# Optimization experiments

Measured on AMD Instinct MI355X. Metric: run time of the kernel, lower is better.

Reference implementation:

```python
import jax, jax.numpy as jnp
import numpy as np

HIDDEN = 2048
N_HEADS = 16
N_KV = 4
HEAD_DIM = 128
SEQ = 2048
BATCH = 2
THETA = 10000.0


def rotate_half(x):
    half = x.shape[-1] // 2
    x1, x2 = x[..., :half], x[..., half:]
    return jnp.concatenate((-x2, x1), axis=-1)


def rope_cos_sin(seq_len, dim, theta, dtype):
    inv_freq = 1.0 / (theta ** (jnp.arange(0, dim, 2, dtype=jnp.float32) / dim))
    t = jnp.arange(seq_len, dtype=jnp.float32)
    freqs = jnp.einsum('i,j->ij', t, inv_freq)            # [S, dim/2]
    emb = jnp.concatenate((freqs, freqs), axis=-1)        # [S, dim]
    return jnp.cos(emb).astype(dtype), jnp.sin(emb).astype(dtype)


def setup_inputs() -> dict:
    key = jax.random.key(0)
    kx, kq, kk, kv, ko = jax.random.split(key, 5)
    s = 0.02
    return {
        'x':  jax.random.normal(kx, (BATCH, SEQ, HIDDEN), dtype=jnp.float32),
        'Wq': jax.random.normal(kq, (HIDDEN, N_HEADS * HEAD_DIM), dtype=jnp.float32) * s,
        'Wk': jax.random.normal(kk, (HIDDEN, N_KV * HEAD_DIM), dtype=jnp.float32) * s,
        'Wv': jax.random.normal(kv, (HIDDEN, N_KV * HEAD_DIM), dtype=jnp.float32) * s,
        'Wo': jax.random.normal(ko, (N_HEADS * HEAD_DIM, HIDDEN), dtype=jnp.float32) * s,
    }


def reference(x, Wq, Wk, Wv, Wo):
    B, S, _ = x.shape
    q = (x @ Wq).reshape(B, S, N_HEADS, HEAD_DIM)
    k = (x @ Wk).reshape(B, S, N_KV, HEAD_DIM)
    v = (x @ Wv).reshape(B, S, N_KV, HEAD_DIM)

    cos, sin = rope_cos_sin(S, HEAD_DIM, THETA, x.dtype)
    cos = cos[None, :, None, :]  # [1,S,1,D]
    sin = sin[None, :, None, :]
    q = q * cos + rotate_half(q) * sin
    k = k * cos + rotate_half(k) * sin

    repeat = N_HEADS // N_KV
    k = jnp.repeat(k, repeat, axis=2)  # repeat_interleave over heads
    v = jnp.repeat(v, repeat, axis=2)

    # [B,H,S,D]
    q = q.transpose(0, 2, 1, 3)
    k = k.transpose(0, 2, 1, 3)
    v = v.transpose(0, 2, 1, 3)

    scale = HEAD_DIM ** -0.5
    scores = jnp.einsum('bhqd,bhkd->bhqk', q, k) * scale
    causal = jnp.triu(jnp.full((S, S), -jnp.inf, dtype=scores.dtype), k=1)
    scores = scores + causal
    probs = jax.nn.softmax(scores, axis=-1)
    out = jnp.einsum('bhqk,bhkd->bhqd', probs, v)
    out = out.transpose(0, 2, 1, 3).reshape(B, S, N_HEADS * HEAD_DIM)
    return out @ Wo
```

## Files before the change

kernel.cpp:

```cpp
#include <hip/hip_runtime.h>
#include <hip/hip_bf16.h>
#include <math.h>

#define HIDDEN 2048
#define NHEADS 16
#define NKV 4
#define HD 128
#define SEQ 2048
#define BATCH 2
#define MTOT (BATCH*SEQ)
#define NQ (NHEADS*HD)
#define NKVD (NKV*HD)
#define NQKV (NQ + 2*NKVD)

typedef __attribute__((ext_vector_type(8))) short short8;
typedef __attribute__((ext_vector_type(4))) float float4v;

#if __has_builtin(__builtin_amdgcn_exp2f)
#define EXP2F __builtin_amdgcn_exp2f
#else
#define EXP2F exp2f
#endif
#define C1 0.1275174f

static __device__ __forceinline__ unsigned short f2bf(float f) {
  union { float f; unsigned int u; } v; v.f = f;
  unsigned int r = v.u + 0x7FFF + ((v.u >> 16) & 1);
  return (unsigned short)(r >> 16);
}
static __device__ __forceinline__ float bf2f(unsigned short h) {
  union { unsigned int u; float f; } v; v.u = ((unsigned int)h) << 16;
  return v.f;
}

static __device__ __forceinline__ void async16(const unsigned short* g, unsigned short* l) {
  __builtin_amdgcn_global_load_lds(
      (const __attribute__((address_space(1))) unsigned int*)g,
      (__attribute__((address_space(3))) unsigned int*)l, 16, 0, 0);
}

__global__ void prep(const float* __restrict__ x, unsigned short* __restrict__ xb,
                     const float* __restrict__ Wq, const float* __restrict__ Wk,
                     const float* __restrict__ Wv, const float* __restrict__ Wo,
                     unsigned short* __restrict__ Wqt, unsigned short* __restrict__ Wkt,
                     unsigned short* __restrict__ Wvt, unsigned short* __restrict__ Wot) {
  __shared__ float tile[32][33];
  int bx = blockIdx.x;
  if (bx < 8192) {
    int i = (bx * 256 + threadIdx.x) * 4;
    float4 v = *(const float4*)(x + i);
    ushort4 o;
    o.x = f2bf(v.x); o.y = f2bf(v.y); o.z = f2bf(v.z); o.w = f2bf(v.w);
    *(ushort4*)(xb + i) = o;
    return;
  }
  int bz = bx - 8192;
  int tbx = bz % 160, tby = bz / 160;
  const int K = 2048;
  const float* W; unsigned short* Wt; int N; int tn;
  if (tbx < 64)      { W = Wq; Wt = Wqt; N = NQ;     tn = tbx * 32; }
  else if (tbx < 80) { W = Wk; Wt = Wkt; N = NKVD;   tn = (tbx - 64) * 32; }
  else if (tbx < 96) { W = Wv; Wt = Wvt; N = NKVD;   tn = (tbx - 80) * 32; }
  else               { W = Wo; Wt = Wot; N = HIDDEN; tn = (tbx - 96) * 32; }
  int tk = tby * 32;
  int tx = threadIdx.x & 31;
  int ty = threadIdx.x >> 5;
  #pragma unroll
  for (int i = 0; i < 4; i++) {
    int k = tk + ty + i * 8;
    tile[ty + i * 8][tx] = W[(size_t)k * N + tn + tx];
  }
  __syncthreads();
  #pragma unroll
  for (int i = 0; i < 4; i++) {
    int n = tn + ty + i * 8;
    Wt[(size_t)n * K + tk + tx] = f2bf(tile[tx][ty + i * 8]);
  }
}

__global__ void rope_k(unsigned short* __restrict__ Kb) {
  int idx = blockIdx.x * blockDim.x + threadIdx.x;
  int d = idx & 63;
  int hr = idx >> 6;
  int spos = (hr / NKV) % SEQ;
  size_t base = (size_t)hr * HD;
  float inv = exp2f((float)d * -0.2076205059304601f);
  float ang = (float)spos * inv;
  float sn, cs;
  sincosf(ang, &sn, &cs);
  float q1 = bf2f(Kb[base + d]);
  float q2 = bf2f(Kb[base + d + 64]);
  Kb[base + d]      = f2bf(q1 * cs - q2 * sn);
  Kb[base + d + 64] = f2bf(q2 * cs + q1 * sn);
}

__global__ __launch_bounds__(1024, 4) void gemm_qkv(
    const unsigned short* __restrict__ A,
    const unsigned short* __restrict__ Bt,
    unsigned short* __restrict__ Qb,
    unsigned short* __restrict__ Kb,
    unsigned short* __restrict__ Vt) {
  __shared__ __align__(16) unsigned short L[4 * 16384];
  const int K = HIDDEN;
  const int NT = K / 32;
  int bm = blockIdx.y * 256, bn = blockIdx.x * 256;
  int tid = threadIdx.x, w = tid >> 6, lane = tid & 63;
  int wrow = w >> 2, wcol = w & 3;
  int m16 = lane & 15, quad = lane >> 4;
  int r = tid >> 2, lch = tid & 3;
  int lchs = lch ^ ((r >> 1) & 3);
  int qx = quad ^ ((m16 >> 1) & 3);
  const unsigned short* Agp = A + (size_t)(bm + r) * K + lchs * 8;
  const unsigned short* Bgp = Bt + (size_t)(bn + r) * K + lchs * 8;

  float4v acc[4][4];
  #pragma unroll
  for (int i = 0; i < 4; i++)
    #pragma unroll
    for (int j = 0; j < 4; j++) acc[i][j] = (float4v)0.0f;

  auto stage = [&](int t) {
    unsigned short* Lb = L + (t & 3) * 16384;
    int k0 = t * 32;
    async16(Agp + k0, Lb + tid * 8);
    async16(Bgp + k0, Lb + 8192 + tid * 8);
  };

  const bool isV = (blockIdx.x >= 10);

  stage(0); stage(1);
  asm volatile("s_waitcnt vmcnt(2)" ::: "memory");
  __builtin_amdgcn_s_barrier();
  __builtin_amdgcn_sched_barrier(0);

  if (!isV) {
    for (int t = 0; t < NT; ++t) {
      if (t + 2 < NT) stage(t + 2);
      const unsigned short* Ab_ = L + (t & 3) * 16384;
      const unsigned short* Bb_ = Ab_ + 8192;
      short8 af[4], bfr[4];
      #pragma unroll
      for (int i = 0; i < 4; i++)
        af[i] = *(const short8*)(&Ab_[(wrow * 64 + i * 16 + m16) * 32 + qx * 8]);
      #pragma unroll
      for (int j = 0; j < 4; j++)
        bfr[j] = *(const short8*)(&Bb_[(wcol * 64 + j * 16 + m16) * 32 + qx * 8]);
      __builtin_amdgcn_s_setprio(1);
      #pragma unroll
      for (int i = 0; i < 4; i++)
        #pragma unroll
        for (int j = 0; j < 4; j++)
          acc[i][j] = __builtin_amdgcn_mfma_f32_16x16x32_bf16(af[i], bfr[j], acc[i][j], 0, 0, 0);
      __builtin_amdgcn_s_setprio(0);
      if (t + 2 < NT) { asm volatile("s_waitcnt vmcnt(2)" ::: "memory"); }
      else            { asm volatile("s_waitcnt vmcnt(0)" ::: "memory"); }
      __builtin_amdgcn_s_barrier();
      __builtin_amdgcn_sched_barrier(0);
    }
  } else {
    for (int t = 0; t < NT; ++t) {
      if (t + 2 < NT) stage(t + 2);
      const unsigned short* Ab_ = L + (t & 3) * 16384;
      const unsigned short* Bb_ = Ab_ + 8192;
      short8 af[4], bfr[4];
      #pragma unroll
      for (int i = 0; i < 4; i++)
        af[i] = *(const short8*)(&Ab_[(wrow * 64 + i * 16 + m16) * 32 + qx * 8]);
      #pragma unroll
      for (int j = 0; j < 4; j++)
        bfr[j] = *(const short8*)(&Bb_[(wcol * 64 + j * 16 + m16) * 32 + qx * 8]);
      __builtin_amdgcn_s_setprio(1);
      #pragma unroll
      for (int i = 0; i < 4; i++)
        #pragma unroll
        for (int j = 0; j < 4; j++)
          acc[i][j] = __builtin_amdgcn_mfma_f32_16x16x32_bf16(bfr[j], af[i], acc[i][j], 0, 0, 0);
      __builtin_amdgcn_s_setprio(0);
      if (t + 2 < NT) { asm volatile("s_waitcnt vmcnt(2)" ::: "memory"); }
      else            { asm volatile("s_waitcnt vmcnt(0)" ::: "memory"); }
      __builtin_amdgcn_s_barrier();
      __builtin_amdgcn_sched_barrier(0);
    }
  }

  if (blockIdx.x < 8) {
    #pragma unroll
    for (int i = 0; i < 4; i++)
      #pragma unroll
      for (int j = 0; j < 4; j++)
        #pragma unroll
        for (int rr = 0; rr < 4; rr++) {
          int row = bm + wrow * 64 + i * 16 + quad * 4 + rr;
          int col = bn + wcol * 64 + j * 16 + m16;
          Qb[(size_t)row * NQ + col] = f2bf(acc[i][j][rr]);
        }
  } else if (!isV) {
    #pragma unroll
    for (int i = 0; i < 4; i++)
      #pragma unroll
      for (int j = 0; j < 4; j++)
        #pragma unroll
        for (int rr = 0; rr < 4; rr++) {
          int row = bm + wrow * 64 + i * 16 + quad * 4 + rr;
          int col = bn - 2048 + wcol * 64 + j * 16 + m16;
          Kb[(size_t)row * NKVD + col] = f2bf(acc[i][j][rr]);
        }
  } else {
    #pragma unroll
    for (int i = 0; i < 4; i++)
      #pragma unroll
      for (int j = 0; j < 4; j++)
        #pragma unroll
        for (int rr = 0; rr < 4; rr++) {
          int f = bn - 2560 + wcol * 64 + j * 16 + quad * 4 + rr;
          int m = bm + wrow * 64 + i * 16 + m16;
          Vt[(size_t)f * MTOT + m] = f2bf(acc[i][j][rr]);
        }
  }
}

__global__ __launch_bounds__(512, 4) void gemm_o(
    const unsigned short* __restrict__ A,
    const unsigned short* __restrict__ Bt,
    float* __restrict__ C, int M, int N, int K) {
  __shared__ __align__(16) unsigned short L[4 * 8192];
  const int NT = K / 32;
  int bm = blockIdx.y * 128, bn = blockIdx.x * 128;
  int tid = threadIdx.x, w = tid >> 6, lane = tid & 63;
  int wrow = w >> 2, wcol = w & 3;
  int m16 = lane & 15, quad = lane >> 4;
  int r = tid >> 2, lch = tid & 3;
  int lchs = lch ^ ((r >> 1) & 3);
  int qx = quad ^ ((m16 >> 1) & 3);
  const unsigned short* Agp = A + (size_t)(bm + r) * K + lchs * 8;
  const unsigned short* Bgp = Bt + (size_t)(bn + r) * K + lchs * 8;

  float4v acc[4][2];
  #pragma unroll
  for (int i = 0; i < 4; i++)
    #pragma unroll
    for (int j = 0; j < 2; j++) acc[i][j] = (float4v)0.0f;

  auto stage = [&](int t) {
    unsigned short* Lb = L + (t & 3) * 8192;
    int k0 = t * 32;
    async16(Agp + k0, Lb + tid * 8);
    async16(Bgp + k0, Lb + 4096 + tid * 8);
  };

  stage(0); stage(1);
  asm volatile("s_waitcnt vmcnt(2)" ::: "memory");
  __builtin_amdgcn_s_barrier();
  __builtin_amdgcn_sched_barrier(0);

  for (int t = 0; t < NT; ++t) {
    if (t + 2 < NT) stage(t + 2);
    const unsigned short* Ab_ = L + (t & 3) * 8192;
    const unsigned short* Bb_ = Ab_ + 4096;
    short8 af[4], bfr[2];
    #pragma unroll
    for (int i = 0; i < 4; i++)
      af[i] = *(const short8*)(&Ab_[(wrow * 64 + i * 16 + m16) * 32 + qx * 8]);
    #pragma unroll
    for (int j = 0; j < 2; j++)
      bfr[j] = *(const short8*)(&Bb_[(wcol * 32 + j * 16 + m16) * 32 + qx * 8]);
    __builtin_amdgcn_s_setprio(1);
    #pragma unroll
    for (int i = 0; i < 4; i++)
      #pragma unroll
      for (int j = 0; j < 2; j++)
        acc[i][j] = __builtin_amdgcn_mfma_f32_16x16x32_bf16(af[i], bfr[j], acc[i][j], 0, 0, 0);
    __builtin_amdgcn_s_setprio(0);
    if (t + 2 < NT) { asm volatile("s_waitcnt vmcnt(2)" ::: "memory"); }
    else            { asm volatile("s_waitcnt vmcnt(0)" ::: "memory"); }
    __builtin_amdgcn_s_barrier();
    __builtin_amdgcn_sched_barrier(0);
  }

  #pragma unroll
  for (int i = 0; i < 4; i++)
    #pragma unroll
    for (int j = 0; j < 2; j++)
      #pragma unroll
      for (int rr = 0; rr < 4; rr++) {
        int row = bm + wrow * 64 + i * 16 + quad * 4 + rr;
        int col = bn + wcol * 32 + j * 16 + m16;
        C[(size_t)row * N + col] = acc[i][j][rr];
      }
}

#define FLASH_TILE(CUR, NXT)                                                  \
  {                                                                           \
    const int ktb = kt * 64;                                                  \
    __syncthreads();        \
    {                                                                         \
      const unsigned short* Vg = Vt + vgrow * (size_t)MTOT                    \
                                    + (size_t)b * SEQ + ktb + kcv * 32 + vlch * 8; \
      unsigned short* Vl = Vs + kcv * 4096 + ipv * 512;                       \
      _Pragma("unroll")                                                       \
      for (int i = 0; i < 4; i++) async16(Vg + (size_t)i * 16 * MTOT, Vl + i * 512); \
    }                                                                         \
    if (kt < H) {                                                             \
      const unsigned short* Kg = Kp + (((size_t)b * SEQ + (kt + 1) * 64 + lrow) * NKV + kvh) * HD + w * 32 + vlch * 8; \
      unsigned short* Kl = NXT + w * 2048;                                    \
      _Pragma("unroll")                                                       \
      for (int i = 0; i < 4; i++) async16(Kg + (size_t)i * 16 * NKV * HD, Kl + i * 512); \
    }                                                                         \
    const bool act1 = (ktb <= lmax_w);                                        \
    float4v sacc[2][4];                                                       \
    _Pragma("unroll") for (int s4 = 0; s4 < 4; s4++) {                        \
      sacc[0][s4] = (float4v)0.0f; sacc[1][s4] = (float4v)0.0f; }             \
    __builtin_amdgcn_s_setprio(1);                                            \
    if (act1) {                                                               \
      _Pragma("unroll")                                                       \
      for (int s4 = 0; s4 < 4; s4++)                                          \
        _Pragma("unroll")                                                     \
        for (int c = 0; c < 4; c++) {                                         \
          short8 kf = *(const short8*)(&CUR[c * 2048 + (s4 * 16 + m16) * 32 + qx * 8]); \
          sacc[0][s4] = __builtin_amdgcn_mfma_f32_16x16x32_bf16(kf, qf[0][c], sacc[0][s4], 0, 0, 0); \
          sacc[1][s4] = __builtin_amdgcn_mfma_f32_16x16x32_bf16(kf, qf[1][c], sacc[1][s4], 0, 0, 0); \
        }                                                                     \
    } else {                                                                  \
      _Pragma("unroll")                                                       \
      for (int s4 = 0; s4 < 4; s4++)                                          \
        _Pragma("unroll")                                                     \
        for (int c = 0; c < 4; c++) {                                         \
          short8 kf = *(const short8*)(&CUR[c * 2048 + (s4 * 16 + m16) * 32 + qx * 8]); \
          sacc[0][s4] = __builtin_amdgcn_mfma_f32_16x16x32_bf16(kf, qf[0][c], sacc[0][s4], 0, 0, 0); \
        }                                                                     \
    }                                                                         \
    __builtin_amdgcn_s_setprio(0);                                            \
    _Pragma("unroll")                                                         \
    for (int qs = 0; qs < 2; qs++) {                                          \
      if (qs == 0 || act1) {                                                  \
        const int tb = qs ? L : H;                                            \
        const int qabs = tb * 64 + w * 16 + m16;                              \
        const bool diag = (kt == tb);                                         \
        float sv[4][4]; float mloc = -1e30f;                                  \
        if (diag) {                                                           \
          _Pragma("unroll") for (int s4 = 0; s4 < 4; s4++)                    \
            _Pragma("unroll") for (int rr = 0; rr < 4; rr++) {                \
              int kabs = ktb + s4 * 16 + quad * 4 + rr;                       \
              float t = sacc[qs][s4][rr];                                     \
              sv[s4][rr] = (kabs > qabs) ? -1e30f : t;                        \
              mloc = fmaxf(mloc, sv[s4][rr]); }                               \
        } else {                                                              \
          _Pragma("unroll") for (int s4 = 0; s4 < 4; s4++)                    \
            _Pragma("unroll") for (int rr = 0; rr < 4; rr++) {                \
              sv[s4][rr] = sacc[qs][s4][rr]; mloc = fmaxf(mloc, sv[s4][rr]); } \
        }                                                                     \
        mloc *= C1;                                                           \
        mloc = fmaxf(mloc, __shfl_xor(mloc, 16, 64));                         \
        mloc = fmaxf(mloc, __shfl_xor(mloc, 32, 64));                         \
        float mnewS = fmaxf(miS[qs], mloc);                                   \
        const bool defer = (bool)__all(mloc <= miS[qs] + 8.0f);               \
        if (defer) mnewS = miS[qs];  \
        const int prow = qs * 64 + w * 16 + m16;                              \
        const int psw = prow * 32; const int rx = prow & 7;                   \
        float rs = 0.0f;                                                      \
        _Pragma("unroll") for (int s4 = 0; s4 < 4; s4++) {                    \
          float p0 = EXP2F(__builtin_fmaf(sv[s4][0], C1, -mnewS));            \
          float p1 = EXP2F(__builtin_fmaf(sv[s4][1], C1, -mnewS));            \
          float p2 = EXP2F(__builtin_fmaf(sv[s4][2], C1, -mnewS));            \
          float p3 = EXP2F(__builtin_fmaf(sv[s4][3], C1, -mnewS));            \
          rs += p0 + p1 + p2 + p3;                                            \
          uint2 u;                                                            \
          u.x = (__float_as_uint(p1) & 0xffff0000u) | (__float_as_uint(p0) >> 16); \
          u.y = (__float_as_uint(p3) & 0xffff0000u) | (__float_as_uint(p2) >> 16); \
          int chunkW = s4 * 2 + (quad >> 1);                                  \
          *(uint2*)(&Ps[psw + ((chunkW ^ rx) << 2) + (quad & 1) * 2]) = u;    \
        }                                                                     \
        rs += __shfl_xor(rs, 16, 64);                                         \
        rs += __shfl_xor(rs, 32, 64);                                         \
        if (!defer) {                                                         \
          const float alpha = EXP2F(miS[qs] - mnewS);                         \
          li[qs] *= alpha; miS[qs] = mnewS;                                   \
          _Pragma("unroll") for (int ds = 0; ds < 8; ds++) oacc[ds][qs] *= alpha; \
        }                                                                     \
        li[qs] += rs;                                                         \
      }                                                                       \
    }                                                                         \
    __syncthreads();     \
    {                                                                         \
      const int r0 = w * 16 + m16, r1 = 64 + w * 16 + m16;                    \
      __builtin_amdgcn_s_setprio(1);                                          \
      if (act1) {                                                             \
        _Pragma("unroll")                                                     \
        for (int kc = 0; kc < 2; kc++) {                                      \
          short8 pf0 = *(const short8*)(&Ps[r0 * 32 + (((kc * 4 + quad) ^ (r0 & 7)) << 2)]); \
          short8 pf1 = *(const short8*)(&Ps[r1 * 32 + (((kc * 4 + quad) ^ (r1 & 7)) << 2)]); \
          _Pragma("unroll")                                                   \
          for (int ds = 0; ds < 8; ds++) {                                    \
            short8 vf = *(const short8*)(&Vs[kc * 4096 + (ds * 16 + m16) * 32 + qx * 8]); \
            oacc[ds][0] = __builtin_amdgcn_mfma_f32_16x16x32_bf16(vf, pf0, oacc[ds][0], 0, 0, 0); \
            oacc[ds][1] = __builtin_amdgcn_mfma_f32_16x16x32_bf16(vf, pf1, oacc[ds][1], 0, 0, 0); \
          }                                                                   \
        }                                                                     \
      } else {                                                                \
        _Pragma("unroll")                                                     \
        for (int kc = 0; kc < 2; kc++) {                                      \
          short8 pf0 = *(const short8*)(&Ps[r0 * 32 + (((kc * 4 + quad) ^ (r0 & 7)) << 2)]); \
          _Pragma("unroll")                                                   \
          for (int ds = 0; ds < 8; ds++) {                                    \
            short8 vf = *(const short8*)(&Vs[kc * 4096 + (ds * 16 + m16) * 32 + qx * 8]); \
            oacc[ds][0] = __builtin_amdgcn_mfma_f32_16x16x32_bf16(vf, pf0, oacc[ds][0], 0, 0, 0); \
          }                                                                   \
        }                                                                     \
      }                                                                       \
      __builtin_amdgcn_s_setprio(0);                                          \
    }                                                                         \
  }

__global__ __launch_bounds__(256, 2) void flash_attn(
    const unsigned short* __restrict__ Q,
    const unsigned short* __restrict__ Kp,
    const unsigned short* __restrict__ Vt,
    unsigned short* __restrict__ O) {
  __shared__ unsigned short Ks0[4 * 64 * 32];
  __shared__ unsigned short Ks1[4 * 64 * 32];
  __shared__ unsigned short Vs[2 * 128 * 32];
  __shared__ unsigned int   Ps[128 * 32];

  int bx = blockIdx.x;
  int h  = blockIdx.y;
  int b  = blockIdx.z;
  int kvh = h >> 2;
  int H = 31 - bx, L = bx;
  int tid = threadIdx.x;
  int w = tid >> 6, lane = tid & 63;
  int m16 = lane & 15, quad = lane >> 4;
  int lrow = lane >> 2, lch = lane & 3;
  const int vlch = lch ^ ((lrow >> 1) & 3);
  const int qx = quad ^ ((m16 >> 1) & 3);
  const int lmax_w = L * 64 + w * 16 + 15;

  const int kcv = w >> 1, ipv = (w & 1) * 4;
  const size_t vgrow = (size_t)kvh * HD + ipv * 16 + lrow;

  short8 qf[2][4];
  #pragma unroll
  for (int qs = 0; qs < 2; qs++) {
    int tb = qs ? L : H;
    size_t qbase = (((size_t)b * SEQ + tb * 64 + w * 16 + m16) * NHEADS + h) * HD;
    #pragma unroll
    for (int c = 0; c < 4; c++)
      qf[qs][c] = *(const short8*)(Q + qbase + c * 32 + quad * 8);
  }
  #pragma unroll
  for (int qs = 0; qs < 2; qs++) {
    int tb = qs ? L : H;
    float spos = (float)(tb * 64 + w * 16 + m16);
    #pragma unroll
    for (int c = 0; c < 2; c++) {
      #pragma unroll
      for (int e = 0; e < 8; e++) {
        int d = c * 32 + quad * 8 + e;
        float inv = exp2f((float)d * -0.2076205059304601f);
        float ang = spos * inv;
        float sn, cs;
        sincosf(ang, &sn, &cs);
        float f1 = bf2f((unsigned short)qf[qs][c][e]);
        float f2 = bf2f((unsigned short)qf[qs][c + 2][e]);
        qf[qs][c][e]     = (short)f2bf(f1 * cs - f2 * sn);
        qf[qs][c + 2][e] = (short)f2bf(f2 * cs + f1 * sn);
      }
    }
  }

  float4v oacc[8][2];
  #pragma unroll
  for (int ds = 0; ds < 8; ds++) { oacc[ds][0] = (float4v)0.0f; oacc[ds][1] = (float4v)0.0f; }
  float miS[2] = {-1e30f, -1e30f}, li[2] = {0.0f, 0.0f};

  {
    const unsigned short* Kg = Kp + (((size_t)b * SEQ + lrow) * NKV + kvh) * HD + w * 32 + vlch * 8;
    unsigned short* Kl = Ks0 + w * 2048;
    #pragma unroll
    for (int i = 0; i < 4; i++) async16(Kg + (size_t)i * 16 * NKV * HD, Kl + i * 512);
  }

  int kt = 0;
  for (;;) {
    FLASH_TILE(Ks0, Ks1)
    if (++kt > H) break;
    FLASH_TILE(Ks1, Ks0)
    if (++kt > H) break;
  }

  #pragma unroll
  for (int qs = 0; qs < 2; qs++) {
    float inv = 1.0f / li[qs];
    int tb = qs ? L : H;
    int qabs = tb * 64 + w * 16 + m16;
    size_t obase = (((size_t)b * SEQ + qabs) * NHEADS + h) * HD + quad * 4;
    #pragma unroll
    for (int ds = 0; ds < 8; ds++) {
      float v0 = oacc[ds][qs][0] * inv;
      float v1 = oacc[ds][qs][1] * inv;
      float v2 = oacc[ds][qs][2] * inv;
      float v3 = oacc[ds][qs][3] * inv;
      uint2 u;
      u.x = ((unsigned)f2bf(v1) << 16) | f2bf(v0);
      u.y = ((unsigned)f2bf(v3) << 16) | f2bf(v2);
      *(uint2*)(O + obase + ds * 16) = u;
    }
  }
}

extern "C" void kernel_launch(void* const* d_in, const int* in_sizes, int n_in,
                              void* d_out, int out_size, void* d_ws, size_t ws_size,
                              hipStream_t stream) {
  const float* x  = (const float*)d_in[0];
  const float* Wq = (const float*)d_in[1];
  const float* Wk = (const float*)d_in[2];
  const float* Wv = (const float*)d_in[3];
  const float* Wo = (const float*)d_in[4];
  float* out = (float*)d_out;

  unsigned short* ws = (unsigned short*)d_ws;
  unsigned short* xb  = ws;
  unsigned short* Wqt = xb  + (size_t)MTOT * HIDDEN;
  unsigned short* Wkt = Wqt + (size_t)NQ * HIDDEN;
  unsigned short* Wvt = Wkt + (size_t)NKVD * HIDDEN;
  unsigned short* Wot = Wvt + (size_t)NKVD * HIDDEN;
  unsigned short* Qb  = Wot + (size_t)NQ * HIDDEN;
  unsigned short* Kb  = Qb  + (size_t)MTOT * NQ;
  unsigned short* Vtb = Kb  + (size_t)MTOT * NKVD;
  unsigned short* Ab  = Vtb + (size_t)MTOT * NKVD;

  prep<<<8192 + 160 * 64, 256, 0, stream>>>(x, xb, Wq, Wk, Wv, Wo, Wqt, Wkt, Wvt, Wot);

  gemm_qkv<<<dim3(NQKV / 256, MTOT / 256), 1024, 0, stream>>>(xb, Wqt, Qb, Kb, Vtb);

  rope_k<<<(MTOT * NKV * 64) / 256, 256, 0, stream>>>(Kb);

  flash_attn<<<dim3(16, NHEADS, BATCH), 256, 0, stream>>>(Qb, Kb, Vtb, Ab);

  gemm_o<<<dim3(HIDDEN / 128, MTOT / 128), 512, 0, stream>>>(Ab, Wot, out, MTOT, HIDDEN, NQ);
}
```

Measured before the change: 276.1 us.

## Fuse K RoPE into QKV GEMM epilogue with head-wide wave tiling

```diff
diff --git a/kernel.cpp b/kernel.cpp
--- a/kernel.cpp
+++ b/kernel.cpp
@@ -78,22 +78,6 @@
   }
 }
 
-__global__ void rope_k(unsigned short* __restrict__ Kb) {
-  int idx = blockIdx.x * blockDim.x + threadIdx.x;
-  int d = idx & 63;
-  int hr = idx >> 6;
-  int spos = (hr / NKV) % SEQ;
-  size_t base = (size_t)hr * HD;
-  float inv = exp2f((float)d * -0.2076205059304601f);
-  float ang = (float)spos * inv;
-  float sn, cs;
-  sincosf(ang, &sn, &cs);
-  float q1 = bf2f(Kb[base + d]);
-  float q2 = bf2f(Kb[base + d + 64]);
-  Kb[base + d]      = f2bf(q1 * cs - q2 * sn);
-  Kb[base + d + 64] = f2bf(q2 * cs + q1 * sn);
-}
-
 __global__ __launch_bounds__(1024, 4) void gemm_qkv(
     const unsigned short* __restrict__ A,
     const unsigned short* __restrict__ Bt,
@@ -105,7 +89,6 @@
   const int NT = K / 32;
   int bm = blockIdx.y * 256, bn = blockIdx.x * 256;
   int tid = threadIdx.x, w = tid >> 6, lane = tid & 63;
-  int wrow = w >> 2, wcol = w & 3;
   int m16 = lane & 15, quad = lane >> 4;
   int r = tid >> 2, lch = tid & 3;
   int lchs = lch ^ ((r >> 1) & 3);
@@ -113,12 +96,6 @@
   const unsigned short* Agp = A + (size_t)(bm + r) * K + lchs * 8;
   const unsigned short* Bgp = Bt + (size_t)(bn + r) * K + lchs * 8;
 
-  float4v acc[4][4];
-  #pragma unroll
-  for (int i = 0; i < 4; i++)
-    #pragma unroll
-    for (int j = 0; j < 4; j++) acc[i][j] = (float4v)0.0f;
-
   auto stage = [&](int t) {
     unsigned short* Lb = L + (t & 3) * 16384;
     int k0 = t * 32;
@@ -127,13 +104,68 @@
   };
 
   const bool isV = (blockIdx.x >= 10);
+  const bool isK = (blockIdx.x >= 8 && blockIdx.x < 10);
 
   stage(0); stage(1);
   asm volatile("s_waitcnt vmcnt(2)" ::: "memory");
   __builtin_amdgcn_s_barrier();
   __builtin_amdgcn_sched_barrier(0);
 
-  if (!isV) {
+  if (isK) {
+    int wrow2 = w >> 1, wcol2 = w & 1;
+    float4v acc[2][8];
+    #pragma unroll
+    for (int i = 0; i < 2; i++)
+      #pragma unroll
+      for (int j = 0; j < 8; j++) acc[i][j] = (float4v)0.0f;
+    for (int t = 0; t < NT; ++t) {
+      if (t + 2 < NT) stage(t + 2);
+      const unsigned short* Ab_ = L + (t & 3) * 16384;
+      const unsigned short* Bb_ = Ab_ + 8192;
+      short8 af[2], bfr[8];
+      #pragma unroll
+      for (int i = 0; i < 2; i++)
+        af[i] = *(const short8*)(&Ab_[(wrow2 * 32 + i * 16 + m16) * 32 + qx * 8]);
+      #pragma unroll
+      for (int j = 0; j < 8; j++)
+        bfr[j] = *(const short8*)(&Bb_[(wcol2 * 128 + j * 16 + m16) * 32 + qx * 8]);
+      __builtin_amdgcn_s_setprio(1);
+      #pragma unroll
+      for (int i = 0; i < 2; i++)
+        #pragma unroll
+        for (int j = 0; j < 8; j++)
+          acc[i][j] = __builtin_amdgcn_mfma_f32_16x16x32_bf16(af[i], bfr[j], acc[i][j], 0, 0, 0);
+      __builtin_amdgcn_s_setprio(0);
+      if (t + 2 < NT) { asm volatile("s_waitcnt vmcnt(2)" ::: "memory"); }
+      else            { asm volatile("s_waitcnt vmcnt(0)" ::: "memory"); }
+      __builtin_amdgcn_s_barrier();
+      __builtin_amdgcn_sched_barrier(0);
+    }
+    #pragma unroll
+    for (int i = 0; i < 2; i++)
+      #pragma unroll
+      for (int rr = 0; rr < 4; rr++) {
+        int row = bm + wrow2 * 32 + i * 16 + quad * 4 + rr;
+        float spos = (float)(row & (SEQ - 1));
+        #pragma unroll
+        for (int j = 0; j < 4; j++) {
+          int d = j * 16 + m16;
+          float inv = exp2f((float)d * -0.2076205059304601f);
+          float sn, cs;
+          sincosf(spos * inv, &sn, &cs);
+          float f1 = acc[i][j][rr], f2 = acc[i][j + 4][rr];
+          int col = (bn - 2048) + wcol2 * 128 + j * 16 + m16;
+          Kb[(size_t)row * NKVD + col]      = f2bf(f1 * cs - f2 * sn);
+          Kb[(size_t)row * NKVD + col + 64] = f2bf(f2 * cs + f1 * sn);
+        }
+      }
+  } else if (!isV) {
+    int wrow = w >> 2, wcol = w & 3;
+    float4v acc[4][4];
+    #pragma unroll
+    for (int i = 0; i < 4; i++)
+      #pragma unroll
+      for (int j = 0; j < 4; j++) acc[i][j] = (float4v)0.0f;
     for (int t = 0; t < NT; ++t) {
       if (t + 2 < NT) stage(t + 2);
       const unsigned short* Ab_ = L + (t & 3) * 16384;
@@ -157,7 +189,23 @@
       __builtin_amdgcn_s_barrier();
       __builtin_amdgcn_sched_barrier(0);
     }
+    #pragma unroll
+    for (int i = 0; i < 4; i++)
+      #pragma unroll
+      for (int j = 0; j < 4; j++)
+        #pragma unroll
+        for (int rr = 0; rr < 4; rr++) {
+          int row = bm + wrow * 64 + i * 16 + quad * 4 + rr;
+          int col = bn + wcol * 64 + j * 16 + m16;
+          Qb[(size_t)row * NQ + col] = f2bf(acc[i][j][rr]);
+        }
   } else {
+    int wrow = w >> 2, wcol = w & 3;
+    float4v acc[4][4];
+    #pragma unroll
+    for (int i = 0; i < 4; i++)
+      #pragma unroll
+      for (int j = 0; j < 4; j++) acc[i][j] = (float4v)0.0f;
     for (int t = 0; t < NT; ++t) {
       if (t + 2 < NT) stage(t + 2);
       const unsigned short* Ab_ = L + (t & 3) * 16384;
@@ -181,31 +229,6 @@
       __builtin_amdgcn_s_barrier();
       __builtin_amdgcn_sched_barrier(0);
     }
-  }
-
-  if (blockIdx.x < 8) {
-    #pragma unroll
-    for (int i = 0; i < 4; i++)
-      #pragma unroll
-      for (int j = 0; j < 4; j++)
-        #pragma unroll
-        for (int rr = 0; rr < 4; rr++) {
-          int row = bm + wrow * 64 + i * 16 + quad * 4 + rr;
-          int col = bn + wcol * 64 + j * 16 + m16;
-          Qb[(size_t)row * NQ + col] = f2bf(acc[i][j][rr]);
-        }
-  } else if (!isV) {
-    #pragma unroll
-    for (int i = 0; i < 4; i++)
-      #pragma unroll
-      for (int j = 0; j < 4; j++)
-        #pragma unroll
-        for (int rr = 0; rr < 4; rr++) {
-          int row = bm + wrow * 64 + i * 16 + quad * 4 + rr;
-          int col = bn - 2048 + wcol * 64 + j * 16 + m16;
-          Kb[(size_t)row * NKVD + col] = f2bf(acc[i][j][rr]);
-        }
-  } else {
     #pragma unroll
     for (int i = 0; i < 4; i++)
       #pragma unroll
@@ -532,8 +555,6 @@
 
   gemm_qkv<<<dim3(NQKV / 256, MTOT / 256), 1024, 0, stream>>>(xb, Wqt, Qb, Kb, Vtb);
 
-  rope_k<<<(MTOT * NKV * 64) / 256, 256, 0, stream>>>(Kb);
-
   flash_attn<<<dim3(16, NHEADS, BATCH), 256, 0, stream>>>(Qb, Kb, Vtb, Ab);
 
   gemm_o<<<dim3(HIDDEN / 128, MTOT / 128), 512, 0, stream>>>(Ab, Wot, out, MTOT, HIDDEN, NQ);
```

New measurement: 283.1 us. 2.5% more time.
